# Performance work log

Hardware: AMD Instinct MI355X
Metric: run time of the kernel (lower is better)

## Reference

```python
import jax, jax.numpy as jnp
import numpy as np

N_NODES = 50000
N_EDGES = 800000
HIDDEN = 256          # hidden_size == output_size (same `inputs` feeds all projections)
NUM_HEADS = 8
D_K = HIDDEN // NUM_HEADS  # 32
SCALE = float(np.sqrt(D_K))


def setup_inputs() -> dict:
    key = jax.random.key(0)
    ks = jax.random.split(key, 8)
    w_std = 1.0 / np.sqrt(HIDDEN)
    inputs = jax.random.normal(ks[0], (N_NODES, HIDDEN), jnp.float32)
    src = jax.random.randint(ks[1], (N_EDGES,), 0, N_NODES, dtype=jnp.int32)
    # guarantee every node has >= 1 in-edge (avoid 0/0 in normalization)
    dst_rand = jax.random.randint(ks[2], (N_EDGES - N_NODES,), 0, N_NODES, dtype=jnp.int32)
    dst = jnp.concatenate([jnp.arange(N_NODES, dtype=jnp.int32), dst_rand])
    Wq = jax.random.normal(ks[3], (HIDDEN, HIDDEN), jnp.float32) * w_std
    bq = jnp.zeros((HIDDEN,), jnp.float32)
    Wk = jax.random.normal(ks[4], (HIDDEN, HIDDEN), jnp.float32) * w_std
    Wv = jax.random.normal(ks[5], (HIDDEN, HIDDEN), jnp.float32) * w_std
    Wo = jax.random.normal(ks[6], (HIDDEN, HIDDEN), jnp.float32) * w_std
    bo = jnp.zeros((HIDDEN,), jnp.float32)
    return {"inputs": inputs, "Wq": Wq, "bq": bq, "Wk": Wk, "Wv": Wv,
            "Wo": Wo, "bo": bo, "src": src, "dst": dst}


def reference(inputs, Wq, bq, Wk, Wv, Wo, bo, src, dst):
    n = inputs.shape[0]
    # projections (dropout is identity in eval mode)
    q = (inputs @ Wq.T + bq).reshape(n, NUM_HEADS, D_K)
    k = (inputs @ Wk.T).reshape(n, NUM_HEADS, D_K)
    v = (inputs @ Wv.T).reshape(n, NUM_HEADS, D_K)
    # edge-wise dot product score: k[src] . q[dst]  -> [E, H]
    score = jnp.einsum('ehd,ehd->eh', k[src], q[dst])
    score = jnp.exp(jnp.clip(score / SCALE, -10.0, 10.0))
    # weighted segment-sum aggregation over in-edges of each dst node
    wv = jax.ops.segment_sum(v[src] * score[..., None], dst, num_segments=n)  # [N,H,dk]
    z = jax.ops.segment_sum(score, dst, num_segments=n)                        # [N,H]
    o = (wv / z[..., None]).reshape(n, HIDDEN)
    return o @ Wo.T + bo
```

## Files before the change

### kernel.cpp

```cpp
#include <hip/hip_runtime.h>
#include <hip/hip_bf16.h>
#include <math.h>

#define HIDDEN 256
#define INV_SCALE 0.17677669529663687f

typedef __attribute__((ext_vector_type(8))) short short8;
typedef __attribute__((ext_vector_type(4))) float f32x4;
typedef const __attribute__((address_space(1))) unsigned int* gas_ptr;
typedef __attribute__((address_space(3))) unsigned int* las_ptr;

static __device__ __forceinline__ unsigned short f2bf(float x) {
  unsigned u = __float_as_uint(x);
  unsigned r = (u + 0x7FFF + ((u >> 16) & 1)) >> 16;
  return (unsigned short)r;
}
static __device__ __forceinline__ float bf2f(unsigned short u) {
  return __uint_as_float((unsigned)u << 16);
}


__global__ __launch_bounds__(256) void conv_a_kernel(const float* __restrict__ in,
                                                     unsigned short* __restrict__ out,
                                                     int total4) {
  int stride = gridDim.x * blockDim.x;
  for (int i = blockIdx.x * blockDim.x + threadIdx.x; i < total4; i += stride) {
    float4 f = ((const float4*)in)[i];
    ushort4 u;
    u.x = f2bf(f.x); u.y = f2bf(f.y); u.z = f2bf(f.z); u.w = f2bf(f.w);
    ((ushort4*)out)[i] = u;
  }
}

__global__ __launch_bounds__(256) void conv_w_kernel(const float* __restrict__ Wq,
                                                     const float* __restrict__ Wk,
                                                     const float* __restrict__ Wv,
                                                     const float* __restrict__ Wo,
                                                     unsigned short* __restrict__ wqkv,
                                                     unsigned short* __restrict__ wob) {
  int i = blockIdx.x * 256 + threadIdx.x;
  int m = i >> 16;
  int j = i & 65535;
  const float* s = (m == 0) ? Wq : (m == 1) ? Wk : (m == 2) ? Wv : Wo;
  unsigned short b = f2bf(s[j]);
  if (m < 3) wqkv[m * 65536 + j] = b;
  else wob[j] = b;
}


__global__ __launch_bounds__(256) void hist_kernel(const int* __restrict__ dst,
                                                   int* __restrict__ deg, int E) {
  int e = blockIdx.x * blockDim.x + threadIdx.x;
  if (e < E) atomicAdd(&deg[dst[e]], 1);
}

__global__ __launch_bounds__(256) void scan1_kernel(const int* __restrict__ deg,
                                                    int* __restrict__ offs,
                                                    int* __restrict__ bsums, int N) {
  __shared__ int s[256];
  int tid = threadIdx.x;
  int base = blockIdx.x * 1024 + tid * 4;
  int v0 = (base + 0 < N) ? deg[base + 0] : 0;
  int v1 = (base + 1 < N) ? deg[base + 1] : 0;
  int v2 = (base + 2 < N) ? deg[base + 2] : 0;
  int v3 = (base + 3 < N) ? deg[base + 3] : 0;
  int tsum = v0 + v1 + v2 + v3;
  s[tid] = tsum;
  __syncthreads();
  for (int off = 1; off < 256; off <<= 1) {
    int t = (tid >= off) ? s[tid - off] : 0;
    __syncthreads();
    s[tid] += t;
    __syncthreads();
  }
  int excl = s[tid] - tsum;
  if (base + 0 < N) offs[base + 0] = excl;
  if (base + 1 < N) offs[base + 1] = excl + v0;
  if (base + 2 < N) offs[base + 2] = excl + v0 + v1;
  if (base + 3 < N) offs[base + 3] = excl + v0 + v1 + v2;
  if (tid == 255) bsums[blockIdx.x] = s[255];
}

__global__ void scan2_kernel(int* __restrict__ bsums, int nb) {
  if (blockIdx.x == 0 && threadIdx.x == 0) {
    int run = 0;
    for (int b = 0; b < nb; ++b) { int t = bsums[b]; bsums[b] = run; run += t; }
  }
}

__global__ __launch_bounds__(256) void scan3_kernel(int* __restrict__ offs,
                                                    int* __restrict__ cursor,
                                                    const int* __restrict__ bsums,
                                                    int N, int E) {
  int i = blockIdx.x * blockDim.x + threadIdx.x;
  if (i < N) {
    int v = offs[i] + bsums[i >> 10];
    offs[i] = v;
    cursor[i] = v;
  }
  if (i == 0) offs[N] = E;
}

__global__ __launch_bounds__(256) void scatter_kernel(const int* __restrict__ dst,
                                                      const int* __restrict__ src,
                                                      int* __restrict__ cursor,
                                                      int* __restrict__ esrc, int E) {
  int e = blockIdx.x * blockDim.x + threadIdx.x;
  if (e < E) {
    int n = dst[e];
    int pos = atomicAdd(&cursor[n], 1);
    esrc[pos] = src[e];
  }
}

#define GBM 128
#define GBN 128
#define GBK 32

template <int MODE>
__global__ __launch_bounds__(256) void mfma_gemm_kernel(const unsigned short* __restrict__ A,
                                                        const unsigned short* __restrict__ B,
                                                        const float* __restrict__ bias,
                                                        float* __restrict__ Cf,
                                                        unsigned short* __restrict__ Ck,
                                                        unsigned short* __restrict__ Cv,
                                                        int M) {
  __shared__ unsigned short As[GBM][GBK];
  __shared__ unsigned short Bs[GBN][GBK];
  int tid = threadIdx.x;
  int lane = tid & 63;
  int wid = tid >> 6;
  int wm = wid >> 1, wn = wid & 1;
  int brow = blockIdx.x * GBM;
  int bcol = blockIdx.y * GBN;

  int srow = wid * 32 + (lane >> 2);
  int skoff = (lane & 3) * 8;
  const unsigned short* gA0 = &A[(size_t)(brow + srow) * HIDDEN + skoff];
  const unsigned short* gA1 = gA0 + (size_t)16 * HIDDEN;
  const unsigned short* gB0 = &B[(size_t)(bcol + srow) * HIDDEN + skoff];
  const unsigned short* gB1 = gB0 + (size_t)16 * HIDDEN;
  char* ldsA = (char*)&As[0][0] + wid * 2048;
  char* ldsB = (char*)&Bs[0][0] + wid * 2048;

  f32x4 acc[4][4] = {};

  int fr = lane & 15;
  int kg = (lane >> 4) * 8;

  for (int k0 = 0; k0 < HIDDEN; k0 += GBK) {
    __syncthreads();
    __builtin_amdgcn_global_load_lds((gas_ptr)(const void*)(gA0 + k0), (las_ptr)(void*)ldsA, 16, 0, 0);
    __builtin_amdgcn_global_load_lds((gas_ptr)(const void*)(gA1 + k0), (las_ptr)(void*)(ldsA + 1024), 16, 0, 0);
    __builtin_amdgcn_global_load_lds((gas_ptr)(const void*)(gB0 + k0), (las_ptr)(void*)ldsB, 16, 0, 0);
    __builtin_amdgcn_global_load_lds((gas_ptr)(const void*)(gB1 + k0), (las_ptr)(void*)(ldsB + 1024), 16, 0, 0);
    asm volatile("s_waitcnt vmcnt(0)" ::: "memory");
    __syncthreads();
    short8 af[4], bfg[4];
#pragma unroll
    for (int mi = 0; mi < 4; ++mi)
      af[mi] = *(const short8*)&As[wm * 64 + mi * 16 + fr][kg];
#pragma unroll
    for (int ni = 0; ni < 4; ++ni)
      bfg[ni] = *(const short8*)&Bs[wn * 64 + ni * 16 + fr][kg];
#pragma unroll
    for (int mi = 0; mi < 4; ++mi)
#pragma unroll
      for (int ni = 0; ni < 4; ++ni)
        acc[mi][ni] = __builtin_amdgcn_mfma_f32_16x16x32_bf16(af[mi], bfg[ni], acc[mi][ni], 0, 0, 0);
  }

  int fq = lane >> 4;
#pragma unroll
  for (int mi = 0; mi < 4; ++mi) {
#pragma unroll
    for (int ni = 0; ni < 4; ++ni) {
      int c = bcol + wn * 64 + ni * 16 + fr;
#pragma unroll
      for (int j = 0; j < 4; ++j) {
        int r = brow + wm * 64 + mi * 16 + fq * 4 + j;
        if (r < M) {
          float val = acc[mi][ni][j];
          if (MODE == 1) {
            Cf[(size_t)r * HIDDEN + c] = val + bias[c];
          } else {
            if (c < 256) Cf[(size_t)r * HIDDEN + c] = val + bias[c];
            else if (c < 512) Ck[(size_t)r * HIDDEN + (c - 256)] = f2bf(val);
            else Cv[(size_t)r * HIDDEN + (c - 512)] = f2bf(val);
          }
        }
      }
    }
  }
}

__global__ __launch_bounds__(256) void agg_kernel(const float* __restrict__ q,
                                                  const unsigned short* __restrict__ k,
                                                  const unsigned short* __restrict__ v,
                                                  const int* __restrict__ offs,
                                                  const int* __restrict__ esrc,
                                                  unsigned short* __restrict__ o, int N) {
  int n = blockIdx.x * 4 + (threadIdx.x >> 6);
  if (n >= N) return;
  int t = threadIdx.x & 63;
  float4 qv = *(const float4*)&q[(size_t)n * HIDDEN + t * 4];
  int e0 = offs[n], e1 = offs[n + 1];
  float w0 = 0.f, w1 = 0.f, w2 = 0.f, w3 = 0.f, z = 0.f;
  int idx = e0;
  for (; idx + 2 <= e1; idx += 2) {
    int sa = esrc[idx], sb = esrc[idx + 1];
    ushort4 ka = *(const ushort4*)&k[(size_t)sa * HIDDEN + t * 4];
    ushort4 kb = *(const ushort4*)&k[(size_t)sb * HIDDEN + t * 4];
    ushort4 va = *(const ushort4*)&v[(size_t)sa * HIDDEN + t * 4];
    ushort4 vb = *(const ushort4*)&v[(size_t)sb * HIDDEN + t * 4];
    float pa = qv.x * bf2f(ka.x) + qv.y * bf2f(ka.y) + qv.z * bf2f(ka.z) + qv.w * bf2f(ka.w);
    float pb = qv.x * bf2f(kb.x) + qv.y * bf2f(kb.y) + qv.z * bf2f(kb.z) + qv.w * bf2f(kb.w);
    pa += __shfl_xor(pa, 4); pb += __shfl_xor(pb, 4);
    pa += __shfl_xor(pa, 2); pb += __shfl_xor(pb, 2);
    pa += __shfl_xor(pa, 1); pb += __shfl_xor(pb, 1);
    float ea = __expf(fminf(fmaxf(pa * INV_SCALE, -10.f), 10.f));
    float eb = __expf(fminf(fmaxf(pb * INV_SCALE, -10.f), 10.f));
    w0 += ea * bf2f(va.x) + eb * bf2f(vb.x);
    w1 += ea * bf2f(va.y) + eb * bf2f(vb.y);
    w2 += ea * bf2f(va.z) + eb * bf2f(vb.z);
    w3 += ea * bf2f(va.w) + eb * bf2f(vb.w);
    z += ea + eb;
  }
  if (idx < e1) {
    int sa = esrc[idx];
    ushort4 ka = *(const ushort4*)&k[(size_t)sa * HIDDEN + t * 4];
    ushort4 va = *(const ushort4*)&v[(size_t)sa * HIDDEN + t * 4];
    float pa = qv.x * bf2f(ka.x) + qv.y * bf2f(ka.y) + qv.z * bf2f(ka.z) + qv.w * bf2f(ka.w);
    pa += __shfl_xor(pa, 4);
    pa += __shfl_xor(pa, 2);
    pa += __shfl_xor(pa, 1);
    float ea = __expf(fminf(fmaxf(pa * INV_SCALE, -10.f), 10.f));
    w0 += ea * bf2f(va.x);
    w1 += ea * bf2f(va.y);
    w2 += ea * bf2f(va.z);
    w3 += ea * bf2f(va.w);
    z += ea;
  }
  float inv = 1.0f / z;
  ushort4 out;
  out.x = f2bf(w0 * inv); out.y = f2bf(w1 * inv);
  out.z = f2bf(w2 * inv); out.w = f2bf(w3 * inv);
  *(ushort4*)&o[(size_t)n * HIDDEN + t * 4] = out;
}


extern "C" void kernel_launch(void* const* d_in, const int* in_sizes, int n_in,
                              void* d_out, int out_size, void* d_ws, size_t ws_size,
                              hipStream_t stream) {
  const float* inputs = (const float*)d_in[0];
  const float* Wq = (const float*)d_in[1];
  const float* bq = (const float*)d_in[2];
  const float* Wk = (const float*)d_in[3];
  const float* Wv = (const float*)d_in[4];
  const float* Wo = (const float*)d_in[5];
  const float* bo = (const float*)d_in[6];
  const int* src = (const int*)d_in[7];
  const int* dst = (const int*)d_in[8];

  int N = in_sizes[0] / HIDDEN;
  int E = in_sizes[7];
  int Mpad = N + GBM;

  char* w = (char*)d_ws;
  unsigned short* a_bf = (unsigned short*)w; w += (size_t)Mpad * HIDDEN * 2;
  float* q = (float*)w;                      w += (size_t)N * HIDDEN * 4;
  unsigned short* kb = (unsigned short*)w;   w += (size_t)N * HIDDEN * 2;
  unsigned short* vb = (unsigned short*)w;   w += (size_t)N * HIDDEN * 2;
  unsigned short* ob = (unsigned short*)w;   w += (size_t)Mpad * HIDDEN * 2;
  unsigned short* wqkv = (unsigned short*)w; w += (size_t)768 * HIDDEN * 2;
  unsigned short* wob = (unsigned short*)w;  w += (size_t)256 * HIDDEN * 2;
  int* deg = (int*)w;    w += (size_t)N * 4;
  int* offs = (int*)w;   w += (size_t)(N + 4) * 4;
  int* cursor = (int*)w; w += (size_t)N * 4;
  int* esrc = (int*)w;   w += (size_t)E * 4;
  int* bsums = (int*)w;  w += 256 * 4;

  conv_a_kernel<<<2048, 256, 0, stream>>>(inputs, a_bf, N * (HIDDEN / 4));
  conv_w_kernel<<<1024, 256, 0, stream>>>(Wq, Wk, Wv, Wo, wqkv, wob);

  hipMemsetAsync(deg, 0, (size_t)N * 4, stream);
  int eb = (E + 255) / 256;
  hist_kernel<<<eb, 256, 0, stream>>>(dst, deg, E);
  int nb = (N + 1023) / 1024;
  scan1_kernel<<<nb, 256, 0, stream>>>(deg, offs, bsums, N);
  scan2_kernel<<<1, 64, 0, stream>>>(bsums, nb);
  scan3_kernel<<<(N + 255) / 256, 256, 0, stream>>>(offs, cursor, bsums, N, E);
  scatter_kernel<<<eb, 256, 0, stream>>>(dst, src, cursor, esrc, E);

  dim3 gqkv((N + GBM - 1) / GBM, 768 / GBN);
  mfma_gemm_kernel<0><<<gqkv, 256, 0, stream>>>(a_bf, wqkv, bq, q, kb, vb, N);

  agg_kernel<<<(N + 3) / 4, 256, 0, stream>>>(q, kb, vb, offs, esrc, ob, N);

  dim3 gout((N + GBM - 1) / GBM, 256 / GBN);
  mfma_gemm_kernel<1><<<gout, 256, 0, stream>>>(ob, wob, bo, (float*)d_out, nullptr, nullptr, N);
}
```

Measured before the change: 304.9 us.

## Double-buffer GEMM LDS loads, store Q in bf16, process two edges per wave

The MFMA GEMM now uses two LDS buffers and prefetches the next K-slice with global_load_lds while computing the current one, waiting only on the older loads. Q is written as bf16 instead of fp32, which halves its store and read traffic. The aggregation kernel is restructured so each half-wave handles a different edge, with 8 features per lane and 16-byte K/V loads, and the halves are combined with a cross-half shuffle at the end. This trades a fixed per-wave edge split for wider gathers and shorter reductions, at some extra precision loss on Q.

```diff
diff --git a/kernel.cpp b/kernel.cpp
--- a/kernel.cpp
+++ b/kernel.cpp
@@ -116,17 +116,19 @@
 #define GBM 128
 #define GBN 128
 #define GBK 32
+#define NKSTEP (HIDDEN / GBK)
 
 template <int MODE>
 __global__ __launch_bounds__(256) void mfma_gemm_kernel(const unsigned short* __restrict__ A,
                                                         const unsigned short* __restrict__ B,
                                                         const float* __restrict__ bias,
                                                         float* __restrict__ Cf,
+                                                        unsigned short* __restrict__ Cq,
                                                         unsigned short* __restrict__ Ck,
                                                         unsigned short* __restrict__ Cv,
                                                         int M) {
-  __shared__ unsigned short As[GBM][GBK];
-  __shared__ unsigned short Bs[GBN][GBK];
+  __shared__ unsigned short As[2][GBM][GBK];
+  __shared__ unsigned short Bs[2][GBN][GBK];
   int tid = threadIdx.x;
   int lane = tid & 63;
   int wid = tid >> 6;
@@ -137,37 +139,58 @@
   int srow = wid * 32 + (lane >> 2);
   int skoff = (lane & 3) * 8;
   const unsigned short* gA0 = &A[(size_t)(brow + srow) * HIDDEN + skoff];
-  const unsigned short* gA1 = gA0 + (size_t)16 * HIDDEN;
   const unsigned short* gB0 = &B[(size_t)(bcol + srow) * HIDDEN + skoff];
-  const unsigned short* gB1 = gB0 + (size_t)16 * HIDDEN;
-  char* ldsA = (char*)&As[0][0] + wid * 2048;
-  char* ldsB = (char*)&Bs[0][0] + wid * 2048;
+  char* ldsA0 = (char*)&As[0][0][0] + wid * 2048;
+  char* ldsA1 = (char*)&As[1][0][0] + wid * 2048;
+  char* ldsB0 = (char*)&Bs[0][0][0] + wid * 2048;
+  char* ldsB1 = (char*)&Bs[1][0][0] + wid * 2048;
 
   f32x4 acc[4][4] = {};
 
   int fr = lane & 15;
   int kg = (lane >> 4) * 8;
 
-  for (int k0 = 0; k0 < HIDDEN; k0 += GBK) {
-    __syncthreads();
-    __builtin_amdgcn_global_load_lds((gas_ptr)(const void*)(gA0 + k0), (las_ptr)(void*)ldsA, 16, 0, 0);
-    __builtin_amdgcn_global_load_lds((gas_ptr)(const void*)(gA1 + k0), (las_ptr)(void*)(ldsA + 1024), 16, 0, 0);
-    __builtin_amdgcn_global_load_lds((gas_ptr)(const void*)(gB0 + k0), (las_ptr)(void*)ldsB, 16, 0, 0);
-    __builtin_amdgcn_global_load_lds((gas_ptr)(const void*)(gB1 + k0), (las_ptr)(void*)(ldsB + 1024), 16, 0, 0);
-    asm volatile("s_waitcnt vmcnt(0)" ::: "memory");
-    __syncthreads();
+  {
+    const unsigned short* a = gA0;
+    const unsigned short* b = gB0;
+    __builtin_amdgcn_global_load_lds((gas_ptr)(const void*)a, (las_ptr)(void*)ldsA0, 16, 0, 0);
+    __builtin_amdgcn_global_load_lds((gas_ptr)(const void*)(a + 16 * HIDDEN), (las_ptr)(void*)(ldsA0 + 1024), 16, 0, 0);
+    __builtin_amdgcn_global_load_lds((gas_ptr)(const void*)b, (las_ptr)(void*)ldsB0, 16, 0, 0);
+    __builtin_amdgcn_global_load_lds((gas_ptr)(const void*)(b + 16 * HIDDEN), (las_ptr)(void*)(ldsB0 + 1024), 16, 0, 0);
+  }
+
+#pragma unroll
+  for (int t = 0; t < NKSTEP; ++t) {
+    int p = t & 1;
+    if (t + 1 < NKSTEP) {
+      int k1 = (t + 1) * GBK;
+      const unsigned short* a = gA0 + k1;
+      const unsigned short* b = gB0 + k1;
+      char* dA = p ? ldsA0 : ldsA1;
+      char* dB = p ? ldsB0 : ldsB1;
+      __builtin_amdgcn_global_load_lds((gas_ptr)(const void*)a, (las_ptr)(void*)dA, 16, 0, 0);
+      __builtin_amdgcn_global_load_lds((gas_ptr)(const void*)(a + 16 * HIDDEN), (las_ptr)(void*)(dA + 1024), 16, 0, 0);
+      __builtin_amdgcn_global_load_lds((gas_ptr)(const void*)b, (las_ptr)(void*)dB, 16, 0, 0);
+      __builtin_amdgcn_global_load_lds((gas_ptr)(const void*)(b + 16 * HIDDEN), (las_ptr)(void*)(dB + 1024), 16, 0, 0);
+      asm volatile("s_waitcnt vmcnt(4)" ::: "memory");
+    } else {
+      asm volatile("s_waitcnt vmcnt(0)" ::: "memory");
+    }
+    __builtin_amdgcn_s_barrier();
+    __builtin_amdgcn_sched_barrier(0);
     short8 af[4], bfg[4];
 #pragma unroll
     for (int mi = 0; mi < 4; ++mi)
-      af[mi] = *(const short8*)&As[wm * 64 + mi * 16 + fr][kg];
+      af[mi] = *(const short8*)&As[p][wm * 64 + mi * 16 + fr][kg];
 #pragma unroll
     for (int ni = 0; ni < 4; ++ni)
-      bfg[ni] = *(const short8*)&Bs[wn * 64 + ni * 16 + fr][kg];
+      bfg[ni] = *(const short8*)&Bs[p][wn * 64 + ni * 16 + fr][kg];
 #pragma unroll
     for (int mi = 0; mi < 4; ++mi)
 #pragma unroll
       for (int ni = 0; ni < 4; ++ni)
         acc[mi][ni] = __builtin_amdgcn_mfma_f32_16x16x32_bf16(af[mi], bfg[ni], acc[mi][ni], 0, 0, 0);
+    __builtin_amdgcn_s_barrier();
   }
 
   int fq = lane >> 4;
@@ -184,7 +207,7 @@
           if (MODE == 1) {
             Cf[(size_t)r * HIDDEN + c] = val + bias[c];
           } else {
-            if (c < 256) Cf[(size_t)r * HIDDEN + c] = val + bias[c];
+            if (c < 256) Cq[(size_t)r * HIDDEN + c] = f2bf(val + bias[c]);
             else if (c < 512) Ck[(size_t)r * HIDDEN + (c - 256)] = f2bf(val);
             else Cv[(size_t)r * HIDDEN + (c - 512)] = f2bf(val);
           }
@@ -194,7 +217,7 @@
   }
 }
 
-__global__ __launch_bounds__(256) void agg_kernel(const float* __restrict__ q,
+__global__ __launch_bounds__(256) void agg_kernel(const unsigned short* __restrict__ q,
                                                   const unsigned short* __restrict__ k,
                                                   const unsigned short* __restrict__ v,
                                                   const int* __restrict__ offs,
@@ -202,50 +225,57 @@
                                                   unsigned short* __restrict__ o, int N) {
   int n = blockIdx.x * 4 + (threadIdx.x >> 6);
   if (n >= N) return;
-  int t = threadIdx.x & 63;
-  float4 qv = *(const float4*)&q[(size_t)n * HIDDEN + t * 4];
+  int lane = threadIdx.x & 63;
+  int half = lane >> 5;
+  int l = lane & 31;
+
+  float qf[8];
+  {
+    ushort4 qa = *(const ushort4*)&q[(size_t)n * HIDDEN + l * 8];
+    ushort4 qb = *(const ushort4*)&q[(size_t)n * HIDDEN + l * 8 + 4];
+    qf[0] = bf2f(qa.x); qf[1] = bf2f(qa.y); qf[2] = bf2f(qa.z); qf[3] = bf2f(qa.w);
+    qf[4] = bf2f(qb.x); qf[5] = bf2f(qb.y); qf[6] = bf2f(qb.z); qf[7] = bf2f(qb.w);
+  }
+
   int e0 = offs[n], e1 = offs[n + 1];
-  float w0 = 0.f, w1 = 0.f, w2 = 0.f, w3 = 0.f, z = 0.f;
-  int idx = e0;
-  for (; idx + 2 <= e1; idx += 2) {
-    int sa = esrc[idx], sb = esrc[idx + 1];
-    ushort4 ka = *(const ushort4*)&k[(size_t)sa * HIDDEN + t * 4];
-    ushort4 kb = *(const ushort4*)&k[(size_t)sb * HIDDEN + t * 4];
-    ushort4 va = *(const ushort4*)&v[(size_t)sa * HIDDEN + t * 4];
-    ushort4 vb = *(const ushort4*)&v[(size_t)sb * HIDDEN + t * 4];
-    float pa = qv.x * bf2f(ka.x) + qv.y * bf2f(ka.y) + qv.z * bf2f(ka.z) + qv.w * bf2f(ka.w);
-    float pb = qv.x * bf2f(kb.x) + qv.y * bf2f(kb.y) + qv.z * bf2f(kb.z) + qv.w * bf2f(kb.w);
-    pa += __shfl_xor(pa, 4); pb += __shfl_xor(pb, 4);
-    pa += __shfl_xor(pa, 2); pb += __shfl_xor(pb, 2);
-    pa += __shfl_xor(pa, 1); pb += __shfl_xor(pb, 1);
-    float ea = __expf(fminf(fmaxf(pa * INV_SCALE, -10.f), 10.f));
-    float eb = __expf(fminf(fmaxf(pb * INV_SCALE, -10.f), 10.f));
-    w0 += ea * bf2f(va.x) + eb * bf2f(vb.x);
-    w1 += ea * bf2f(va.y) + eb * bf2f(vb.y);
-    w2 += ea * bf2f(va.z) + eb * bf2f(vb.z);
-    w3 += ea * bf2f(va.w) + eb * bf2f(vb.w);
-    z += ea + eb;
-  }
-  if (idx < e1) {
-    int sa = esrc[idx];
-    ushort4 ka = *(const ushort4*)&k[(size_t)sa * HIDDEN + t * 4];
-    ushort4 va = *(const ushort4*)&v[(size_t)sa * HIDDEN + t * 4];
-    float pa = qv.x * bf2f(ka.x) + qv.y * bf2f(ka.y) + qv.z * bf2f(ka.z) + qv.w * bf2f(ka.w);
-    pa += __shfl_xor(pa, 4);
-    pa += __shfl_xor(pa, 2);
-    pa += __shfl_xor(pa, 1);
-    float ea = __expf(fminf(fmaxf(pa * INV_SCALE, -10.f), 10.f));
-    w0 += ea * bf2f(va.x);
-    w1 += ea * bf2f(va.y);
-    w2 += ea * bf2f(va.z);
-    w3 += ea * bf2f(va.w);
-    z += ea;
-  }
-  float inv = 1.0f / z;
-  ushort4 out;
-  out.x = f2bf(w0 * inv); out.y = f2bf(w1 * inv);
-  out.z = f2bf(w2 * inv); out.w = f2bf(w3 * inv);
-  *(ushort4*)&o[(size_t)n * HIDDEN + t * 4] = out;
+  float wv[8] = {};
+  float z = 0.f;
+
+  for (int idx = e0; idx < e1; idx += 2) {
+    int my = idx + half;
+    bool valid = my < e1;
+    int s = esrc[valid ? my : idx];
+    const ushort4* kp = (const ushort4*)&k[(size_t)s * HIDDEN + l * 8];
+    const ushort4* vp = (const ushort4*)&v[(size_t)s * HIDDEN + l * 8];
+    ushort4 ka = kp[0], kb = kp[1];
+    ushort4 va = vp[0], vb = vp[1];
+    float dot = qf[0] * bf2f(ka.x) + qf[1] * bf2f(ka.y) + qf[2] * bf2f(ka.z) + qf[3] * bf2f(ka.w)
+              + qf[4] * bf2f(kb.x) + qf[5] * bf2f(kb.y) + qf[6] * bf2f(kb.z) + qf[7] * bf2f(kb.w);
+    dot += __shfl_xor(dot, 1);
+    dot += __shfl_xor(dot, 2);
+    float e = 0.f;
+    if (valid) e = __expf(fminf(fmaxf(dot * INV_SCALE, -10.f), 10.f));
+    wv[0] += e * bf2f(va.x); wv[1] += e * bf2f(va.y);
+    wv[2] += e * bf2f(va.z); wv[3] += e * bf2f(va.w);
+    wv[4] += e * bf2f(vb.x); wv[5] += e * bf2f(vb.y);
+    wv[6] += e * bf2f(vb.z); wv[7] += e * bf2f(vb.w);
+    z += e;
+  }
+
+#pragma unroll
+  for (int j = 0; j < 8; ++j) wv[j] += __shfl_xor(wv[j], 32);
+  z += __shfl_xor(z, 32);
+
+  if (half == 0) {
+    float inv = 1.0f / z;
+    ushort4 o0, o1;
+    o0.x = f2bf(wv[0] * inv); o0.y = f2bf(wv[1] * inv);
+    o0.z = f2bf(wv[2] * inv); o0.w = f2bf(wv[3] * inv);
+    o1.x = f2bf(wv[4] * inv); o1.y = f2bf(wv[5] * inv);
+    o1.z = f2bf(wv[6] * inv); o1.w = f2bf(wv[7] * inv);
+    ushort4* op = (ushort4*)&o[(size_t)n * HIDDEN + l * 8];
+    op[0] = o0; op[1] = o1;
+  }
 }
 
 
@@ -268,7 +298,7 @@
 
   char* w = (char*)d_ws;
   unsigned short* a_bf = (unsigned short*)w; w += (size_t)Mpad * HIDDEN * 2;
-  float* q = (float*)w;                      w += (size_t)N * HIDDEN * 4;
+  unsigned short* qb = (unsigned short*)w;   w += (size_t)N * HIDDEN * 2;
   unsigned short* kb = (unsigned short*)w;   w += (size_t)N * HIDDEN * 2;
   unsigned short* vb = (unsigned short*)w;   w += (size_t)N * HIDDEN * 2;
   unsigned short* ob = (unsigned short*)w;   w += (size_t)Mpad * HIDDEN * 2;
@@ -293,10 +323,10 @@
   scatter_kernel<<<eb, 256, 0, stream>>>(dst, src, cursor, esrc, E);
 
   dim3 gqkv((N + GBM - 1) / GBM, 768 / GBN);
-  mfma_gemm_kernel<0><<<gqkv, 256, 0, stream>>>(a_bf, wqkv, bq, q, kb, vb, N);
-
-  agg_kernel<<<(N + 3) / 4, 256, 0, stream>>>(q, kb, vb, offs, esrc, ob, N);
+  mfma_gemm_kernel<0><<<gqkv, 256, 0, stream>>>(a_bf, wqkv, bq, nullptr, qb, kb, vb, N);
+
+  agg_kernel<<<(N + 3) / 4, 256, 0, stream>>>(qb, kb, vb, offs, esrc, ob, N);
 
   dim3 gout((N + GBM - 1) / GBM, 256 / GBN);
-  mfma_gemm_kernel<1><<<gout, 256, 0, stream>>>(ob, wob, bo, (float*)d_out, nullptr, nullptr, N);
-}
+  mfma_gemm_kernel<1><<<gout, 256, 0, stream>>>(ob, wob, bo, (float*)d_out, nullptr, nullptr, nullptr, N);
+}
```

Result: slower. 313.9 us (+3.0%).

## Store Q/K/V head-major in bf16 and aggregate per head with edge-parallel lanes

Applied to the files above, without the earlier changes.

The QKV GEMM now writes Q, K and V as bf16 in a head-major layout ([head][node][32]), so Q shrinks from fp32 to bf16. The aggregation kernel launches one block per (node chunk, head). Each wavefront processes 16 edges at a time, with 4 lanes per edge loading 16-byte pieces, and reduces across lanes at the end. The goal is to make each gathered K/V row for one head a contiguous 64-byte segment, which should improve cache locality per head. The trade-offs are extra shuffle reductions, wasted lanes on low-degree nodes, 8x more blocks, and bf16 rounding of Q.

```diff
diff --git a/kernel.cpp b/kernel.cpp
--- a/kernel.cpp
+++ b/kernel.cpp
@@ -18,6 +18,8 @@
 static __device__ __forceinline__ float bf2f(unsigned short u) {
   return __uint_as_float((unsigned)u << 16);
 }
+
+#define GLL(gp, lp) __builtin_amdgcn_global_load_lds((gas_ptr)(const void*)(gp), (las_ptr)(void*)(lp), 16, 0, 0)
 
 
 __global__ __launch_bounds__(256) void conv_a_kernel(const float* __restrict__ in,
@@ -122,9 +124,10 @@
                                                         const unsigned short* __restrict__ B,
                                                         const float* __restrict__ bias,
                                                         float* __restrict__ Cf,
+                                                        unsigned short* __restrict__ Cq,
                                                         unsigned short* __restrict__ Ck,
                                                         unsigned short* __restrict__ Cv,
-                                                        int M) {
+                                                        int M, int N) {
   __shared__ unsigned short As[GBM][GBK];
   __shared__ unsigned short Bs[GBN][GBK];
   int tid = threadIdx.x;
@@ -137,9 +140,7 @@
   int srow = wid * 32 + (lane >> 2);
   int skoff = (lane & 3) * 8;
   const unsigned short* gA0 = &A[(size_t)(brow + srow) * HIDDEN + skoff];
-  const unsigned short* gA1 = gA0 + (size_t)16 * HIDDEN;
   const unsigned short* gB0 = &B[(size_t)(bcol + srow) * HIDDEN + skoff];
-  const unsigned short* gB1 = gB0 + (size_t)16 * HIDDEN;
   char* ldsA = (char*)&As[0][0] + wid * 2048;
   char* ldsB = (char*)&Bs[0][0] + wid * 2048;
 
@@ -150,10 +151,8 @@
 
   for (int k0 = 0; k0 < HIDDEN; k0 += GBK) {
     __syncthreads();
-    __builtin_amdgcn_global_load_lds((gas_ptr)(const void*)(gA0 + k0), (las_ptr)(void*)ldsA, 16, 0, 0);
-    __builtin_amdgcn_global_load_lds((gas_ptr)(const void*)(gA1 + k0), (las_ptr)(void*)(ldsA + 1024), 16, 0, 0);
-    __builtin_amdgcn_global_load_lds((gas_ptr)(const void*)(gB0 + k0), (las_ptr)(void*)ldsB, 16, 0, 0);
-    __builtin_amdgcn_global_load_lds((gas_ptr)(const void*)(gB1 + k0), (las_ptr)(void*)(ldsB + 1024), 16, 0, 0);
+    GLL(gA0 + k0, ldsA); GLL(gA0 + k0 + 16 * HIDDEN, ldsA + 1024);
+    GLL(gB0 + k0, ldsB); GLL(gB0 + k0 + 16 * HIDDEN, ldsB + 1024);
     asm volatile("s_waitcnt vmcnt(0)" ::: "memory");
     __syncthreads();
     short8 af[4], bfg[4];
@@ -184,9 +183,11 @@
           if (MODE == 1) {
             Cf[(size_t)r * HIDDEN + c] = val + bias[c];
           } else {
-            if (c < 256) Cf[(size_t)r * HIDDEN + c] = val + bias[c];
-            else if (c < 512) Ck[(size_t)r * HIDDEN + (c - 256)] = f2bf(val);
-            else Cv[(size_t)r * HIDDEN + (c - 512)] = f2bf(val);
+            int cc = c & 255;
+            size_t addr = ((size_t)(cc >> 5) * N + r) * 32 + (cc & 31);
+            if (c < 256) Cq[addr] = f2bf(val + bias[c]);
+            else if (c < 512) Ck[addr] = f2bf(val);
+            else Cv[addr] = f2bf(val);
           }
         }
       }
@@ -194,58 +195,64 @@
   }
 }
 
-__global__ __launch_bounds__(256) void agg_kernel(const float* __restrict__ q,
-                                                  const unsigned short* __restrict__ k,
-                                                  const unsigned short* __restrict__ v,
+__global__ __launch_bounds__(256) void agg_kernel(const unsigned short* __restrict__ qh,
+                                                  const unsigned short* __restrict__ kh,
+                                                  const unsigned short* __restrict__ vh,
                                                   const int* __restrict__ offs,
                                                   const int* __restrict__ esrc,
                                                   unsigned short* __restrict__ o, int N) {
-  int n = blockIdx.x * 4 + (threadIdx.x >> 6);
+  int h = blockIdx.x & 7;
+  int chunk = blockIdx.x >> 3;
+  int n = chunk * 4 + (threadIdx.x >> 6);
   if (n >= N) return;
-  int t = threadIdx.x & 63;
-  float4 qv = *(const float4*)&q[(size_t)n * HIDDEN + t * 4];
+  int lane = threadIdx.x & 63;
+  int g = lane >> 2;
+  int cs = (lane & 3) * 8;
+
+  size_t headbase = (size_t)h * N;
+
+  float qf[8];
+  {
+    short8 qv = *(const short8*)&qh[(headbase + n) * 32 + cs];
+#pragma unroll
+    for (int j = 0; j < 8; ++j) qf[j] = bf2f((unsigned short)qv[j]);
+  }
+
   int e0 = offs[n], e1 = offs[n + 1];
-  float w0 = 0.f, w1 = 0.f, w2 = 0.f, w3 = 0.f, z = 0.f;
-  int idx = e0;
-  for (; idx + 2 <= e1; idx += 2) {
-    int sa = esrc[idx], sb = esrc[idx + 1];
-    ushort4 ka = *(const ushort4*)&k[(size_t)sa * HIDDEN + t * 4];
-    ushort4 kb = *(const ushort4*)&k[(size_t)sb * HIDDEN + t * 4];
-    ushort4 va = *(const ushort4*)&v[(size_t)sa * HIDDEN + t * 4];
-    ushort4 vb = *(const ushort4*)&v[(size_t)sb * HIDDEN + t * 4];
-    float pa = qv.x * bf2f(ka.x) + qv.y * bf2f(ka.y) + qv.z * bf2f(ka.z) + qv.w * bf2f(ka.w);
-    float pb = qv.x * bf2f(kb.x) + qv.y * bf2f(kb.y) + qv.z * bf2f(kb.z) + qv.w * bf2f(kb.w);
-    pa += __shfl_xor(pa, 4); pb += __shfl_xor(pb, 4);
-    pa += __shfl_xor(pa, 2); pb += __shfl_xor(pb, 2);
-    pa += __shfl_xor(pa, 1); pb += __shfl_xor(pb, 1);
-    float ea = __expf(fminf(fmaxf(pa * INV_SCALE, -10.f), 10.f));
-    float eb = __expf(fminf(fmaxf(pb * INV_SCALE, -10.f), 10.f));
-    w0 += ea * bf2f(va.x) + eb * bf2f(vb.x);
-    w1 += ea * bf2f(va.y) + eb * bf2f(vb.y);
-    w2 += ea * bf2f(va.z) + eb * bf2f(vb.z);
-    w3 += ea * bf2f(va.w) + eb * bf2f(vb.w);
-    z += ea + eb;
-  }
-  if (idx < e1) {
-    int sa = esrc[idx];
-    ushort4 ka = *(const ushort4*)&k[(size_t)sa * HIDDEN + t * 4];
-    ushort4 va = *(const ushort4*)&v[(size_t)sa * HIDDEN + t * 4];
-    float pa = qv.x * bf2f(ka.x) + qv.y * bf2f(ka.y) + qv.z * bf2f(ka.z) + qv.w * bf2f(ka.w);
-    pa += __shfl_xor(pa, 4);
-    pa += __shfl_xor(pa, 2);
-    pa += __shfl_xor(pa, 1);
-    float ea = __expf(fminf(fmaxf(pa * INV_SCALE, -10.f), 10.f));
-    w0 += ea * bf2f(va.x);
-    w1 += ea * bf2f(va.y);
-    w2 += ea * bf2f(va.z);
-    w3 += ea * bf2f(va.w);
-    z += ea;
-  }
-  float inv = 1.0f / z;
-  ushort4 out;
-  out.x = f2bf(w0 * inv); out.y = f2bf(w1 * inv);
-  out.z = f2bf(w2 * inv); out.w = f2bf(w3 * inv);
-  *(ushort4*)&o[(size_t)n * HIDDEN + t * 4] = out;
+  float wv[8] = {};
+  float z = 0.f;
+
+  for (int b = e0; b < e1; b += 16) {
+    int my = b + g;
+    bool valid = my < e1;
+    int s = esrc[valid ? my : (e1 - 1)];
+    short8 kv = *(const short8*)&kh[(headbase + s) * 32 + cs];
+    short8 vv = *(const short8*)&vh[(headbase + s) * 32 + cs];
+    float d = 0.f;
+#pragma unroll
+    for (int j = 0; j < 8; ++j) d += qf[j] * bf2f((unsigned short)kv[j]);
+    d += __shfl_xor(d, 1);
+    d += __shfl_xor(d, 2);
+    float e = valid ? __expf(fminf(fmaxf(d * INV_SCALE, -10.f), 10.f)) : 0.f;
+#pragma unroll
+    for (int j = 0; j < 8; ++j) wv[j] += e * bf2f((unsigned short)vv[j]);
+    z += e;
+  }
+
+#pragma unroll
+  for (int m = 4; m < 64; m <<= 1) {
+#pragma unroll
+    for (int j = 0; j < 8; ++j) wv[j] += __shfl_xor(wv[j], m);
+    z += __shfl_xor(z, m);
+  }
+
+  if (g == 0) {
+    float inv = 1.0f / z;
+    short8 ov;
+#pragma unroll
+    for (int j = 0; j < 8; ++j) ov[j] = (short)f2bf(wv[j] * inv);
+    *(short8*)&o[(size_t)n * HIDDEN + h * 32 + cs] = ov;
+  }
 }
 
 
@@ -268,9 +275,9 @@
 
   char* w = (char*)d_ws;
   unsigned short* a_bf = (unsigned short*)w; w += (size_t)Mpad * HIDDEN * 2;
-  float* q = (float*)w;                      w += (size_t)N * HIDDEN * 4;
-  unsigned short* kb = (unsigned short*)w;   w += (size_t)N * HIDDEN * 2;
-  unsigned short* vb = (unsigned short*)w;   w += (size_t)N * HIDDEN * 2;
+  unsigned short* qh = (unsigned short*)w;   w += (size_t)N * HIDDEN * 2;
+  unsigned short* kh = (unsigned short*)w;   w += (size_t)N * HIDDEN * 2;
+  unsigned short* vh = (unsigned short*)w;   w += (size_t)N * HIDDEN * 2;
   unsigned short* ob = (unsigned short*)w;   w += (size_t)Mpad * HIDDEN * 2;
   unsigned short* wqkv = (unsigned short*)w; w += (size_t)768 * HIDDEN * 2;
   unsigned short* wob = (unsigned short*)w;  w += (size_t)256 * HIDDEN * 2;
@@ -293,10 +300,11 @@
   scatter_kernel<<<eb, 256, 0, stream>>>(dst, src, cursor, esrc, E);
 
   dim3 gqkv((N + GBM - 1) / GBM, 768 / GBN);
-  mfma_gemm_kernel<0><<<gqkv, 256, 0, stream>>>(a_bf, wqkv, bq, q, kb, vb, N);
-
-  agg_kernel<<<(N + 3) / 4, 256, 0, stream>>>(q, kb, vb, offs, esrc, ob, N);
+  mfma_gemm_kernel<0><<<gqkv, 256, 0, stream>>>(a_bf, wqkv, bq, nullptr, qh, kh, vh, N, N);
+
+  int chunks = (N + 3) / 4;
+  agg_kernel<<<chunks * 8, 256, 0, stream>>>(qh, kh, vh, offs, esrc, ob, N);
 
   dim3 gout((N + GBM - 1) / GBM, 256 / GBN);
-  mfma_gemm_kernel<1><<<gout, 256, 0, stream>>>(ob, wob, bo, (float*)d_out, nullptr, nullptr, N);
-}
+  mfma_gemm_kernel<1><<<gout, 256, 0, stream>>>(ob, wob, bo, (float*)d_out, nullptr, nullptr, nullptr, N, N);
+}
```

Measured after the change: 374.4 us. +22.8%, slower.
